# Kernel optimization log

Hardware: AMD Instinct MI355X
Metric: run time of the kernel (lower is better)

Reference implementation:

```python
import jax, jax.numpy as jnp
import numpy as np

N = 100000   # nodes
E = 1600000  # edges (avg degree 16)
IN = 7       # in_channels
H = 2        # heads
C = 64       # hidden_dim (per-head channels)
NC = 4       # num_classes
SLOPE = 0.2  # PyG GATConv default negative_slope


def gat_layer(x, W, a_src, a_dst, b, src, dst, concat):
    """PyG-style GATConv. x:[n,F], W:[F,H*C], a_*:[H,C], src/dst:[E'] (incl self-loops)."""
    n = x.shape[0]
    h = (x @ W).reshape(n, H, C)                 # [n,H,C]
    es = jnp.sum(h * a_src, axis=-1)             # [n,H] per-node source score
    ed = jnp.sum(h * a_dst, axis=-1)             # [n,H] per-node dest score
    e = jax.nn.leaky_relu(es[src] + ed[dst], SLOPE)          # [E',H]
    m = jax.ops.segment_max(e, dst, num_segments=n)          # stable segment softmax
    p = jnp.exp(e - m[dst])
    s = jax.ops.segment_sum(p, dst, num_segments=n)
    alpha = p / s[dst]                                        # [E',H]
    out = jax.ops.segment_sum(h[src] * alpha[:, :, None], dst, num_segments=n)  # [n,H,C]
    out = out.reshape(n, H * C) if concat else out.mean(axis=1)
    return out + b


def setup_inputs() -> dict:
    key = jax.random.key(0)
    ks = jax.random.split(key, 14)
    sc = 0.2
    return {
        "x": jax.random.normal(ks[0], (N, IN), jnp.float32),
        "edge_index": jax.random.randint(ks[1], (2, E), 0, N, dtype=jnp.int32),
        "W1": jax.random.normal(ks[2], (IN, H * C), jnp.float32) * sc,
        "a_src1": jax.random.normal(ks[3], (H, C), jnp.float32) * sc,
        "a_dst1": jax.random.normal(ks[4], (H, C), jnp.float32) * sc,
        "b1": jnp.zeros((H * C,), jnp.float32),
        "W2": jax.random.normal(ks[5], (H * C, H * C), jnp.float32) * sc,
        "a_src2": jax.random.normal(ks[6], (H, C), jnp.float32) * sc,
        "a_dst2": jax.random.normal(ks[7], (H, C), jnp.float32) * sc,
        "b2": jnp.zeros((C,), jnp.float32),
        "Wc1": jax.random.normal(ks[8], (C, C), jnp.float32) * sc,
        "bc1": jnp.zeros((C,), jnp.float32),
        "Wc2": jax.random.normal(ks[9], (C, NC), jnp.float32) * sc,
        "bc2": jnp.zeros((NC,), jnp.float32),
    }


def reference(x, edge_index, W1, a_src1, a_dst1, b1, W2, a_src2, a_dst2, b2, Wc1, bc1, Wc2, bc2):
    loops = jnp.arange(N, dtype=edge_index.dtype)            # PyG default add_self_loops=True
    src = jnp.concatenate([edge_index[0], loops])
    dst = jnp.concatenate([edge_index[1], loops])
    h = jax.nn.relu(gat_layer(x, W1, a_src1, a_dst1, b1, src, dst, True))   # [N, 128]
    h = gat_layer(h, W2, a_src2, a_dst2, b2, src, dst, False)               # [N, 64]
    return jax.nn.relu(h @ Wc1 + bc1) @ Wc2 + bc2                           # [N, 4]
```

## Files before the change

### kernel.cpp

```cpp
#include <hip/hip_runtime.h>
#include <hip/hip_bf16.h>


#define LRELU_SLOPE 0.2f

__device__ __forceinline__ float wave_red_max(float v) {
#pragma unroll
    for (int o = 32; o > 0; o >>= 1) v = fmaxf(v, __shfl_xor(v, o));
    return v;
}
__device__ __forceinline__ float wave_red_sum(float v) {
#pragma unroll
    for (int o = 32; o > 0; o >>= 1) v += __shfl_xor(v, o);
    return v;
}
__device__ __forceinline__ float lrelu(float v) { return v > 0.f ? v : LRELU_SLOPE * v; }
__device__ __forceinline__ float bf2f(unsigned short u) {
    return __uint_as_float(((unsigned int)u) << 16);
}
__device__ __forceinline__ unsigned short f2bf(float f) {
    unsigned int x = __float_as_uint(f);
    return (unsigned short)((x + 0x7fffu + ((x >> 16) & 1u)) >> 16);
}

__global__ void k_hist(const int* __restrict__ dstA, int* __restrict__ cnt, int E) {
    int i = blockIdx.x * 256 + threadIdx.x;
    if (i < E) atomicAdd(&cnt[dstA[i]], 1);
}

__global__ void k_scan1(const int* __restrict__ cnt, int* __restrict__ rs,
                        int* __restrict__ part, int n) {
    __shared__ int sm[256];
    int t = threadIdx.x;
    int i = blockIdx.x * 256 + t;
    int v = (i < n) ? cnt[i] : 0;
    sm[t] = v;
    __syncthreads();
#pragma unroll
    for (int off = 1; off < 256; off <<= 1) {
        int x = (t >= off) ? sm[t - off] : 0;
        __syncthreads();
        sm[t] += x;
        __syncthreads();
    }
    if (i < n) rs[i] = sm[t] - v;
    if (t == 255) part[blockIdx.x] = sm[255];
}

__global__ void k_scan2(int* part, int np) {
    __shared__ int sm[512];
    int t = threadIdx.x;
    int v = (t < np) ? part[t] : 0;
    sm[t] = v;
    __syncthreads();
#pragma unroll
    for (int off = 1; off < 512; off <<= 1) {
        int x = (t >= off) ? sm[t - off] : 0;
        __syncthreads();
        sm[t] += x;
        __syncthreads();
    }
    if (t < np) part[t] = sm[t] - v;
}

__global__ void k_scan3(int* rs, const int* __restrict__ part, int n, int total) {
    int i = blockIdx.x * 256 + threadIdx.x;
    if (i < n) rs[i] += part[blockIdx.x];
    if (i == 0) rs[n] = total;
}

__global__ void k_scatter(const int* __restrict__ srcA, const int* __restrict__ dstA,
                          const int* __restrict__ rs, int* __restrict__ cur,
                          int* __restrict__ ssrc, int E) {
    int i = blockIdx.x * 256 + threadIdx.x;
    if (i < E) {
        int d = dstA[i];
        int p = atomicAdd(&cur[d], 1);
        ssrc[rs[d] + p] = srcA[i];
    }
}

__global__ void k_prep(const float* __restrict__ W1, const float* __restrict__ as1,
                       const float* __restrict__ ad1, const float* __restrict__ W2,
                       const float* __restrict__ as2, const float* __restrict__ ad2,
                       float* __restrict__ ws1, float* __restrict__ wd1,
                       float* __restrict__ ws2, float* __restrict__ wd2) {
    int t = threadIdx.x;
    int k = t >> 1, h = t & 1;
    float s = 0.f, d = 0.f;
    for (int cc = 0; cc < 64; cc++) {
        float w = W2[k * 128 + h * 64 + cc];
        s += w * as2[h * 64 + cc];
        d += w * ad2[h * 64 + cc];
    }
    ws2[t] = s;
    wd2[t] = d;
    if (t < 14) {
        int kk = t >> 1, hh = t & 1;
        float s1 = 0.f, d1 = 0.f;
        for (int cc = 0; cc < 64; cc++) {
            float w = W1[kk * 128 + hh * 64 + cc];
            s1 += w * as1[hh * 64 + cc];
            d1 += w * ad1[hh * 64 + cc];
        }
        ws1[t] = s1;
        wd1[t] = d1;
    }
}

__global__ void k_feat1(const float* __restrict__ x, const float* __restrict__ W1,
                        const float* __restrict__ ws1, const float* __restrict__ wd1,
                        unsigned short* __restrict__ h1, float* __restrict__ es1,
                        float* __restrict__ ed1, int n) {
    int node = blockIdx.x;
    int c = threadIdx.x;
    float xv[7];
#pragma unroll
    for (int k = 0; k < 7; k++) xv[k] = x[node * 7 + k];
    float acc = 0.f;
#pragma unroll
    for (int k = 0; k < 7; k++) acc += xv[k] * W1[k * 128 + c];
    h1[(size_t)node * 128 + c] = f2bf(acc);
    if (c < 2) {
        float s = 0.f;
#pragma unroll
        for (int k = 0; k < 7; k++) s += xv[k] * ws1[k * 2 + c];
        es1[node * 2 + c] = s;
    } else if (c < 4) {
        int h = c - 2;
        float s = 0.f;
#pragma unroll
        for (int k = 0; k < 7; k++) s += xv[k] * wd1[k * 2 + h];
        ed1[node * 2 + h] = s;
    }
}

template <int LAYER>
__global__ void k_aggr(const unsigned short* __restrict__ h, const float* __restrict__ es,
                       const float* __restrict__ ed, const int* __restrict__ rs,
                       const int* __restrict__ ssrc, const float* __restrict__ bias,
                       float* __restrict__ out, const float* __restrict__ ws2,
                       const float* __restrict__ wd2, float* __restrict__ es2,
                       float* __restrict__ ed2, const float* __restrict__ Wc1,
                       const float* __restrict__ bc1, const float* __restrict__ Wc2,
                       const float* __restrict__ bc2, int n) {
    int wid = threadIdx.x >> 6, lane = threadIdx.x & 63;
    int node = blockIdx.x * 4 + wid;
    if (node >= n) return;
    int beg = rs[node], deg = rs[node + 1] - beg;
    float2 edv = *(const float2*)&ed[node * 2];
    float2 esn = *(const float2*)&es[node * 2];
    float e0s = lrelu(esn.x + edv.x);
    float e1s = lrelu(esn.y + edv.y);
    int head = lane >> 5;
    float accx, accy;

    if (deg <= 64) {
        bool valid = lane < deg;
        int sv = valid ? ssrc[beg + lane] : 0;
        float2 ev;
        ev.x = 0.f; ev.y = 0.f;
        if (valid) ev = *(const float2*)&es[sv * 2];
        float e0 = valid ? lrelu(ev.x + edv.x) : -3.0e38f;
        float e1 = valid ? lrelu(ev.y + edv.y) : -3.0e38f;
        float m0 = fmaxf(wave_red_max(e0), e0s);
        float m1 = fmaxf(wave_red_max(e1), e1s);
        float p0 = valid ? __expf(e0 - m0) : 0.f;
        float p1 = valid ? __expf(e1 - m1) : 0.f;
        float exs0 = __expf(e0s - m0), exs1 = __expf(e1s - m1);
        float inv0 = 1.f / (wave_red_sum(p0) + exs0);
        float inv1 = 1.f / (wave_red_sum(p1) + exs1);
        float a0 = p0 * inv0, a1 = p1 * inv1;
        float aself = head ? exs1 * inv1 : exs0 * inv0;
        ushort2 hvs = *(const ushort2*)&h[(size_t)node * 128 + lane * 2];
        float ax0 = bf2f(hvs.x) * aself, ay0 = bf2f(hvs.y) * aself;
        float ax1 = 0.f, ay1 = 0.f;
        int j = 0;
        for (; j + 8 <= deg; j += 8) {
            int sj[8];
            float aa[8];
#pragma unroll
            for (int q = 0; q < 8; q++) {
                sj[q] = __shfl(sv, j + q);
                float b0 = __shfl(a0, j + q);
                float b1 = __shfl(a1, j + q);
                aa[q] = head ? b1 : b0;
            }
            ushort2 hg[8];
#pragma unroll
            for (int q = 0; q < 8; q++)
                hg[q] = *(const ushort2*)&h[(size_t)sj[q] * 128 + lane * 2];
#pragma unroll
            for (int q = 0; q < 8; q++) {
                float hx = bf2f(hg[q].x), hy = bf2f(hg[q].y);
                if (q & 1) { ax1 += hx * aa[q]; ay1 += hy * aa[q]; }
                else       { ax0 += hx * aa[q]; ay0 += hy * aa[q]; }
            }
        }
        for (; j < deg; j++) {
            int sj = __shfl(sv, j);
            float b0 = __shfl(a0, j), b1 = __shfl(a1, j);
            float aa = head ? b1 : b0;
            ushort2 hh = *(const ushort2*)&h[(size_t)sj * 128 + lane * 2];
            ax0 += bf2f(hh.x) * aa; ay0 += bf2f(hh.y) * aa;
        }
        accx = ax0 + ax1; accy = ay0 + ay1;
    } else {
        float m0 = e0s, s0 = 1.f, m1 = e1s, s1 = 1.f;
        for (int c0 = 0; c0 < deg; c0 += 64) {
            int i = c0 + lane;
            bool val = i < deg;
            int sv = val ? ssrc[beg + i] : 0;
            float e0 = val ? lrelu(es[sv * 2 + 0] + edv.x) : -3.0e38f;
            float e1 = val ? lrelu(es[sv * 2 + 1] + edv.y) : -3.0e38f;
            float nm0 = fmaxf(m0, wave_red_max(e0));
            float nm1 = fmaxf(m1, wave_red_max(e1));
            float p0 = val ? __expf(e0 - nm0) : 0.f;
            float p1 = val ? __expf(e1 - nm1) : 0.f;
            s0 = s0 * __expf(m0 - nm0) + wave_red_sum(p0);
            s1 = s1 * __expf(m1 - nm1) + wave_red_sum(p1);
            m0 = nm0; m1 = nm1;
        }
        float inv0 = 1.f / s0, inv1 = 1.f / s1;
        float aself = head ? __expf(e1s - m1) * inv1 : __expf(e0s - m0) * inv0;
        ushort2 hvs = *(const ushort2*)&h[(size_t)node * 128 + lane * 2];
        accx = bf2f(hvs.x) * aself; accy = bf2f(hvs.y) * aself;
        for (int c0 = 0; c0 < deg; c0 += 64) {
            int i = c0 + lane;
            bool val = i < deg;
            int sv = val ? ssrc[beg + i] : 0;
            float a0 = 0.f, a1 = 0.f;
            if (val) {
                float e0 = lrelu(es[sv * 2 + 0] + edv.x);
                float e1 = lrelu(es[sv * 2 + 1] + edv.y);
                a0 = __expf(e0 - m0) * inv0;
                a1 = __expf(e1 - m1) * inv1;
            }
            int cnt = min(64, deg - c0);
            for (int j = 0; j < cnt; j++) {
                int sj = __shfl(sv, j);
                float b0 = __shfl(a0, j);
                float b1 = __shfl(a1, j);
                float a = head ? b1 : b0;
                ushort2 hh = *(const ushort2*)&h[(size_t)sj * 128 + lane * 2];
                accx += bf2f(hh.x) * a; accy += bf2f(hh.y) * a;
            }
        }
    }

    if (LAYER == 1) {
        float2 bv = *(const float2*)&bias[lane * 2];
        float ox = fmaxf(accx + bv.x, 0.f);
        float oy = fmaxf(accy + bv.y, 0.f);
        float2 o; o.x = ox; o.y = oy;
        *(float2*)&out[(size_t)node * 128 + lane * 2] = o;
        float4 wsv = *(const float4*)&ws2[lane * 4];
        float4 wdv = *(const float4*)&wd2[lane * 4];
        float s0 = ox * wsv.x + oy * wsv.z;
        float s1 = ox * wsv.y + oy * wsv.w;
        float d0 = ox * wdv.x + oy * wdv.z;
        float d1 = ox * wdv.y + oy * wdv.w;
        s0 = wave_red_sum(s0); s1 = wave_red_sum(s1);
        d0 = wave_red_sum(d0); d1 = wave_red_sum(d1);
        if (lane == 0) {
            float2 sv2; sv2.x = s0; sv2.y = s1;
            float2 dv2; dv2.x = d0; dv2.y = d1;
            *(float2*)&es2[node * 2] = sv2;
            *(float2*)&ed2[node * 2] = dv2;
        }
    } else {
        float px = __shfl_xor(accx, 32);
        float py = __shfl_xor(accy, 32);
        int l2 = lane & 31;
        float2 bv = *(const float2*)&bias[l2 * 2];
        float ox = 0.5f * (accx + px) + bv.x;
        float oy = 0.5f * (accy + py) + bv.y;
        float yc0 = bc1[lane], yc1 = 0.f;
#pragma unroll
        for (int q = 0; q < 32; q += 2) {
            float vx0 = __shfl(ox, q), vy0 = __shfl(oy, q);
            float vx1 = __shfl(ox, q + 1), vy1 = __shfl(oy, q + 1);
            yc0 += vx0 * Wc1[(2 * q) * 64 + lane] + vy0 * Wc1[(2 * q + 1) * 64 + lane];
            yc1 += vx1 * Wc1[(2 * q + 2) * 64 + lane] + vy1 * Wc1[(2 * q + 3) * 64 + lane];
        }
        float y = fmaxf(yc0 + yc1, 0.f);
        float4 w2v = *(const float4*)&Wc2[lane * 4];
        float p0 = y * w2v.x, p1 = y * w2v.y, p2 = y * w2v.z, p3 = y * w2v.w;
        p0 = wave_red_sum(p0); p1 = wave_red_sum(p1);
        p2 = wave_red_sum(p2); p3 = wave_red_sum(p3);
        if (lane == 0) {
            float4 o; o.x = p0 + bc2[0]; o.y = p1 + bc2[1];
            o.z = p2 + bc2[2]; o.w = p3 + bc2[3];
            *(float4*)&out[(size_t)node * 4] = o;
        }
    }
}

__global__ void k_gemm2(const float* __restrict__ A, const float* __restrict__ B,
                        unsigned short* __restrict__ C, int M) {
    __shared__ float As[32][65];
    __shared__ float Bs[32][132];
    int bm = blockIdx.x * 64;
    int t = threadIdx.x;
    int tx = t & 31;
    int ty = t >> 5;
    float acc[8][4];
#pragma unroll
    for (int i = 0; i < 8; i++)
#pragma unroll
        for (int j = 0; j < 4; j++) acc[i][j] = 0.f;

    for (int k0 = 0; k0 < 128; k0 += 32) {
        int lk = t & 31, lm = t >> 5;
#pragma unroll
        for (int p = 0; p < 8; p++) {
            int m = lm + p * 8;
            int row = bm + m;
            As[lk][m] = (row < M) ? A[(size_t)row * 128 + k0 + lk] : 0.f;
        }
        int bn = t & 127, bk = t >> 7;
#pragma unroll
        for (int p = 0; p < 16; p++) {
            Bs[bk + p * 2][bn] = B[(k0 + bk + p * 2) * 128 + bn];
        }
        __syncthreads();
#pragma unroll
        for (int k = 0; k < 32; k++) {
            float a[8];
#pragma unroll
            for (int i = 0; i < 8; i++) a[i] = As[k][ty * 8 + i];
            float4 bv = *(const float4*)&Bs[k][tx * 4];
            float b[4] = {bv.x, bv.y, bv.z, bv.w};
#pragma unroll
            for (int i = 0; i < 8; i++)
#pragma unroll
                for (int j = 0; j < 4; j++) acc[i][j] += a[i] * b[j];
        }
        __syncthreads();
    }
#pragma unroll
    for (int i = 0; i < 8; i++) {
        int row = bm + ty * 8 + i;
        if (row < M) {
            ushort4 v;
            v.x = f2bf(acc[i][0]); v.y = f2bf(acc[i][1]);
            v.z = f2bf(acc[i][2]); v.w = f2bf(acc[i][3]);
            *(ushort4*)&C[(size_t)row * 128 + tx * 4] = v;
        }
    }
}

extern "C" void kernel_launch(void* const* d_in, const int* in_sizes, int n_in,
                              void* d_out, int out_size, void* d_ws, size_t ws_size,
                              hipStream_t stream) {
    const float* x   = (const float*)d_in[0];
    const int*   ei  = (const int*)d_in[1];
    const float* W1  = (const float*)d_in[2];
    const float* as1 = (const float*)d_in[3];
    const float* ad1 = (const float*)d_in[4];
    const float* b1  = (const float*)d_in[5];
    const float* W2  = (const float*)d_in[6];
    const float* as2 = (const float*)d_in[7];
    const float* ad2 = (const float*)d_in[8];
    const float* b2  = (const float*)d_in[9];
    const float* Wc1 = (const float*)d_in[10];
    const float* bc1 = (const float*)d_in[11];
    const float* Wc2 = (const float*)d_in[12];
    const float* bc2 = (const float*)d_in[13];
    float* out = (float*)d_out;

    int n = in_sizes[0] / 7;
    int E = in_sizes[1] / 2;
    const int* srcA = ei;
    const int* dstA = ei + E;

    char* ws = (char*)d_ws;
    size_t off = 0;
    auto alloc = [&](size_t bytes) -> char* {
        char* p = ws + off;
        off += (bytes + 255) & ~(size_t)255;
        return p;
    };
    unsigned short* bufH = (unsigned short*)alloc((size_t)n * 128 * 2);
    float* bufO = (float*)alloc((size_t)n * 128 * 4);
    float* es1  = (float*)alloc((size_t)n * 2 * 4);
    float* ed1  = (float*)alloc((size_t)n * 2 * 4);
    float* es2  = (float*)alloc((size_t)n * 2 * 4);
    float* ed2  = (float*)alloc((size_t)n * 2 * 4);
    float* ws1  = (float*)alloc(64);
    float* wd1  = (float*)alloc(64);
    float* ws2v = (float*)alloc(256 * 4);
    float* wd2v = (float*)alloc(256 * 4);
    int* rs   = (int*)alloc((size_t)(n + 1) * 4);
    int* cnt  = (int*)alloc((size_t)n * 4);
    int* part = (int*)alloc(512 * 4);
    int* ssrc = (int*)alloc((size_t)E * 4);

    int eb = (E + 255) / 256;
    int nb = (n + 255) / 256;

    hipMemsetAsync(cnt, 0, (size_t)n * 4, stream);
    k_hist<<<eb, 256, 0, stream>>>(dstA, cnt, E);
    k_scan1<<<nb, 256, 0, stream>>>(cnt, rs, part, n);
    k_scan2<<<1, 512, 0, stream>>>(part, nb);
    k_scan3<<<nb, 256, 0, stream>>>(rs, part, n, E);
    hipMemsetAsync(cnt, 0, (size_t)n * 4, stream);
    k_scatter<<<eb, 256, 0, stream>>>(srcA, dstA, rs, cnt, ssrc, E);

    k_prep<<<1, 256, 0, stream>>>(W1, as1, ad1, W2, as2, ad2, ws1, wd1, ws2v, wd2v);
    k_feat1<<<n, 128, 0, stream>>>(x, W1, ws1, wd1, bufH, es1, ed1, n);
    k_aggr<1><<<(n + 3) / 4, 256, 0, stream>>>(bufH, es1, ed1, rs, ssrc, b1, bufO,
                                               ws2v, wd2v, es2, ed2,
                                               nullptr, nullptr, nullptr, nullptr, n);
    k_gemm2<<<(n + 63) / 64, 256, 0, stream>>>(bufO, W2, bufH, n);
    k_aggr<2><<<(n + 3) / 4, 256, 0, stream>>>(bufH, es2, ed2, rs, ssrc, b2, out,
                                               nullptr, nullptr, nullptr, nullptr,
                                               Wc1, bc1, Wc2, bc2, n);
}
```

Before: 623.7 us.

## Gather neighbor rows with 16-byte loads, four edges in parallel per wave

```diff
diff --git a/kernel.cpp b/kernel.cpp
--- a/kernel.cpp
+++ b/kernel.cpp
@@ -15,12 +15,19 @@
     return v;
 }
 __device__ __forceinline__ float lrelu(float v) { return v > 0.f ? v : LRELU_SLOPE * v; }
-__device__ __forceinline__ float bf2f(unsigned short u) {
-    return __uint_as_float(((unsigned int)u) << 16);
-}
 __device__ __forceinline__ unsigned short f2bf(float f) {
     unsigned int x = __float_as_uint(f);
     return (unsigned short)((x + 0x7fffu + ((x >> 16) & 1u)) >> 16);
+}
+__device__ __forceinline__ void fma8(float* f, uint4 hv, float a) {
+    unsigned u[4] = {hv.x, hv.y, hv.z, hv.w};
+#pragma unroll
+    for (int i = 0; i < 4; i++) {
+        float lo = __uint_as_float(u[i] << 16);
+        float hi = __uint_as_float(u[i] & 0xffff0000u);
+        f[2 * i]     += lo * a;
+        f[2 * i + 1] += hi * a;
+    }
 }
 
 __global__ void k_hist(const int* __restrict__ dstA, int* __restrict__ cnt, int E) {
@@ -147,19 +154,20 @@
     int wid = threadIdx.x >> 6, lane = threadIdx.x & 63;
     int node = blockIdx.x * 4 + wid;
     if (node >= n) return;
+    int grp = lane >> 4, sub = lane & 15;
+    int base = sub * 8;
+    int hd = sub >> 3;
     int beg = rs[node], deg = rs[node + 1] - beg;
     float2 edv = *(const float2*)&ed[node * 2];
     float2 esn = *(const float2*)&es[node * 2];
     float e0s = lrelu(esn.x + edv.x);
     float e1s = lrelu(esn.y + edv.y);
-    int head = lane >> 5;
-    float accx, accy;
+    float f[8] = {0.f, 0.f, 0.f, 0.f, 0.f, 0.f, 0.f, 0.f};
 
     if (deg <= 64) {
         bool valid = lane < deg;
         int sv = valid ? ssrc[beg + lane] : 0;
-        float2 ev;
-        ev.x = 0.f; ev.y = 0.f;
+        float2 ev; ev.x = 0.f; ev.y = 0.f;
         if (valid) ev = *(const float2*)&es[sv * 2];
         float e0 = valid ? lrelu(ev.x + edv.x) : -3.0e38f;
         float e1 = valid ? lrelu(ev.y + edv.y) : -3.0e38f;
@@ -171,40 +179,32 @@
         float inv0 = 1.f / (wave_red_sum(p0) + exs0);
         float inv1 = 1.f / (wave_red_sum(p1) + exs1);
         float a0 = p0 * inv0, a1 = p1 * inv1;
-        float aself = head ? exs1 * inv1 : exs0 * inv0;
-        ushort2 hvs = *(const ushort2*)&h[(size_t)node * 128 + lane * 2];
-        float ax0 = bf2f(hvs.x) * aself, ay0 = bf2f(hvs.y) * aself;
-        float ax1 = 0.f, ay1 = 0.f;
+        if (grp == 0) {
+            float aself = hd ? exs1 * inv1 : exs0 * inv0;
+            uint4 hvs = *(const uint4*)&h[(size_t)node * 128 + base];
+            fma8(f, hvs, aself);
+        }
         int j = 0;
         for (; j + 8 <= deg; j += 8) {
-            int sj[8];
-            float aa[8];
-#pragma unroll
-            for (int q = 0; q < 8; q++) {
-                sj[q] = __shfl(sv, j + q);
-                float b0 = __shfl(a0, j + q);
-                float b1 = __shfl(a1, j + q);
-                aa[q] = head ? b1 : b0;
-            }
-            ushort2 hg[8];
-#pragma unroll
-            for (int q = 0; q < 8; q++)
-                hg[q] = *(const ushort2*)&h[(size_t)sj[q] * 128 + lane * 2];
-#pragma unroll
-            for (int q = 0; q < 8; q++) {
-                float hx = bf2f(hg[q].x), hy = bf2f(hg[q].y);
-                if (q & 1) { ax1 += hx * aa[q]; ay1 += hy * aa[q]; }
-                else       { ax0 += hx * aa[q]; ay0 += hy * aa[q]; }
-            }
-        }
-        for (; j < deg; j++) {
-            int sj = __shfl(sv, j);
-            float b0 = __shfl(a0, j), b1 = __shfl(a1, j);
-            float aa = head ? b1 : b0;
-            ushort2 hh = *(const ushort2*)&h[(size_t)sj * 128 + lane * 2];
-            ax0 += bf2f(hh.x) * aa; ay0 += bf2f(hh.y) * aa;
-        }
-        accx = ax0 + ax1; accy = ay0 + ay1;
+            int jj0 = j + grp, jj1 = j + 4 + grp;
+            int s0v = __shfl(sv, jj0), s1v = __shfl(sv, jj1);
+            float b00 = __shfl(a0, jj0), b10 = __shfl(a1, jj0);
+            float b01 = __shfl(a0, jj1), b11 = __shfl(a1, jj1);
+            float av0 = hd ? b10 : b00;
+            float av1 = hd ? b11 : b01;
+            uint4 h0 = *(const uint4*)&h[(size_t)s0v * 128 + base];
+            uint4 h1 = *(const uint4*)&h[(size_t)s1v * 128 + base];
+            fma8(f, h0, av0);
+            fma8(f, h1, av1);
+        }
+        for (; j < deg; j += 4) {
+            int jj = j + grp;
+            int sjv = __shfl(sv, jj);
+            float b0 = __shfl(a0, jj), b1 = __shfl(a1, jj);
+            float av = hd ? b1 : b0;
+            uint4 hv = *(const uint4*)&h[(size_t)sjv * 128 + base];
+            fma8(f, hv, av);
+        }
     } else {
         float m0 = e0s, s0 = 1.f, m1 = e1s, s1 = 1.f;
         for (int c0 = 0; c0 < deg; c0 += 64) {
@@ -222,46 +222,62 @@
             m0 = nm0; m1 = nm1;
         }
         float inv0 = 1.f / s0, inv1 = 1.f / s1;
-        float aself = head ? __expf(e1s - m1) * inv1 : __expf(e0s - m0) * inv0;
-        ushort2 hvs = *(const ushort2*)&h[(size_t)node * 128 + lane * 2];
-        accx = bf2f(hvs.x) * aself; accy = bf2f(hvs.y) * aself;
+        if (grp == 0) {
+            float aself = hd ? __expf(e1s - m1) * inv1 : __expf(e0s - m0) * inv0;
+            uint4 hvs = *(const uint4*)&h[(size_t)node * 128 + base];
+            fma8(f, hvs, aself);
+        }
         for (int c0 = 0; c0 < deg; c0 += 64) {
             int i = c0 + lane;
             bool val = i < deg;
-            int sv = val ? ssrc[beg + i] : 0;
-            float a0 = 0.f, a1 = 0.f;
+            int svc = val ? ssrc[beg + i] : 0;
+            float a0c = 0.f, a1c = 0.f;
             if (val) {
-                float e0 = lrelu(es[sv * 2 + 0] + edv.x);
-                float e1 = lrelu(es[sv * 2 + 1] + edv.y);
-                a0 = __expf(e0 - m0) * inv0;
-                a1 = __expf(e1 - m1) * inv1;
+                float e0 = lrelu(es[svc * 2 + 0] + edv.x);
+                float e1 = lrelu(es[svc * 2 + 1] + edv.y);
+                a0c = __expf(e0 - m0) * inv0;
+                a1c = __expf(e1 - m1) * inv1;
             }
             int cnt = min(64, deg - c0);
-            for (int j = 0; j < cnt; j++) {
-                int sj = __shfl(sv, j);
-                float b0 = __shfl(a0, j);
-                float b1 = __shfl(a1, j);
-                float a = head ? b1 : b0;
-                ushort2 hh = *(const ushort2*)&h[(size_t)sj * 128 + lane * 2];
-                accx += bf2f(hh.x) * a; accy += bf2f(hh.y) * a;
+            for (int jl = 0; jl < cnt; jl += 4) {
+                int jj = jl + grp;
+                int sjv = __shfl(svc, jj);
+                float b0 = __shfl(a0c, jj), b1 = __shfl(a1c, jj);
+                float av = hd ? b1 : b0;
+                uint4 hv = *(const uint4*)&h[(size_t)sjv * 128 + base];
+                fma8(f, hv, av);
             }
         }
     }
 
+#pragma unroll
+    for (int r = 0; r < 8; r++) {
+        f[r] += __shfl_xor(f[r], 16);
+        f[r] += __shfl_xor(f[r], 32);
+    }
+
     if (LAYER == 1) {
-        float2 bv = *(const float2*)&bias[lane * 2];
-        float ox = fmaxf(accx + bv.x, 0.f);
-        float oy = fmaxf(accy + bv.y, 0.f);
-        float2 o; o.x = ox; o.y = oy;
-        *(float2*)&out[(size_t)node * 128 + lane * 2] = o;
-        float4 wsv = *(const float4*)&ws2[lane * 4];
-        float4 wdv = *(const float4*)&wd2[lane * 4];
-        float s0 = ox * wsv.x + oy * wsv.z;
-        float s1 = ox * wsv.y + oy * wsv.w;
-        float d0 = ox * wdv.x + oy * wdv.z;
-        float d1 = ox * wdv.y + oy * wdv.w;
-        s0 = wave_red_sum(s0); s1 = wave_red_sum(s1);
-        d0 = wave_red_sum(d0); d1 = wave_red_sum(d1);
+        float o[8];
+#pragma unroll
+        for (int r = 0; r < 8; r++) o[r] = fmaxf(f[r] + bias[base + r], 0.f);
+        if (grp == 0) {
+            float4 v0 = {o[0], o[1], o[2], o[3]};
+            float4 v1 = {o[4], o[5], o[6], o[7]};
+            *(float4*)&out[(size_t)node * 128 + base] = v0;
+            *(float4*)&out[(size_t)node * 128 + base + 4] = v1;
+        }
+        float s0 = 0.f, s1 = 0.f, d0 = 0.f, d1 = 0.f;
+#pragma unroll
+        for (int r = 0; r < 8; r++) {
+            float2 wsv = *(const float2*)&ws2[(base + r) * 2];
+            float2 wdv = *(const float2*)&wd2[(base + r) * 2];
+            s0 += o[r] * wsv.x; s1 += o[r] * wsv.y;
+            d0 += o[r] * wdv.x; d1 += o[r] * wdv.y;
+        }
+        s0 = wave_red_sum(s0) * 0.25f;
+        s1 = wave_red_sum(s1) * 0.25f;
+        d0 = wave_red_sum(d0) * 0.25f;
+        d1 = wave_red_sum(d1) * 0.25f;
         if (lane == 0) {
             float2 sv2; sv2.x = s0; sv2.y = s1;
             float2 dv2; dv2.x = d0; dv2.y = d1;
@@ -269,21 +285,20 @@
             *(float2*)&ed2[node * 2] = dv2;
         }
     } else {
-        float px = __shfl_xor(accx, 32);
-        float py = __shfl_xor(accy, 32);
-        int l2 = lane & 31;
-        float2 bv = *(const float2*)&bias[l2 * 2];
-        float ox = 0.5f * (accx + px) + bv.x;
-        float oy = 0.5f * (accy + py) + bv.y;
-        float yc0 = bc1[lane], yc1 = 0.f;
-#pragma unroll
-        for (int q = 0; q < 32; q += 2) {
-            float vx0 = __shfl(ox, q), vy0 = __shfl(oy, q);
-            float vx1 = __shfl(ox, q + 1), vy1 = __shfl(oy, q + 1);
-            yc0 += vx0 * Wc1[(2 * q) * 64 + lane] + vy0 * Wc1[(2 * q + 1) * 64 + lane];
-            yc1 += vx1 * Wc1[(2 * q + 2) * 64 + lane] + vy1 * Wc1[(2 * q + 3) * 64 + lane];
-        }
-        float y = fmaxf(yc0 + yc1, 0.f);
+        float p[8];
+#pragma unroll
+        for (int r = 0; r < 8; r++) p[r] = __shfl_xor(f[r], 8);
+        float o2[8];
+#pragma unroll
+        for (int r = 0; r < 8; r++)
+            o2[r] = 0.5f * (f[r] + p[r]) + bias[(base & 63) + r];
+        float yc = bc1[lane];
+#pragma unroll
+        for (int k = 0; k < 64; k++) {
+            float ov = __shfl(o2[k & 7], k >> 3);
+            yc += ov * Wc1[k * 64 + lane];
+        }
+        float y = fmaxf(yc, 0.f);
         float4 w2v = *(const float4*)&Wc2[lane * 4];
         float p0 = y * w2v.x, p1 = y * w2v.y, p2 = y * w2v.z, p3 = y * w2v.w;
         p0 = wave_red_sum(p0); p1 = wave_red_sum(p1);
```

Measured after the change: 603.5 us. 1.03x faster.
